# Optimization experiments

Hardware: AMD Instinct MI355X
Metric: run time of the kernel (lower is better)

The kernel has to match this reference:

```python
import jax, jax.numpy as jnp
import numpy as np
import math

D_MODEL = 1024
N_HEADS = 16
HEAD_DIM = 64
BATCH = 2
SEQ = 2048


def setup_inputs() -> dict:
    key = jax.random.key(0)
    ks = jax.random.split(key, 5)
    x = jax.random.normal(ks[0], (BATCH, SEQ, D_MODEL), dtype=jnp.float32)
    s = 0.02
    wq = jax.random.normal(ks[1], (D_MODEL, D_MODEL), dtype=jnp.float32) * s
    wk = jax.random.normal(ks[2], (D_MODEL, D_MODEL), dtype=jnp.float32) * s
    wv = jax.random.normal(ks[3], (D_MODEL, D_MODEL), dtype=jnp.float32) * s
    wo = jax.random.normal(ks[4], (D_MODEL, D_MODEL), dtype=jnp.float32) * s
    gammas = jnp.linspace(0.9, 0.99, N_HEADS, dtype=jnp.float32)
    return {"x": x, "wq": wq, "wk": wk, "wv": wv, "wo": wo, "gammas": gammas}


def _decay_mask(length: int, gammas: jnp.ndarray, dtype) -> jnp.ndarray:
    # [H, L, L]: gamma^(t-s) for t >= s, else 0 (causal exponential decay)
    pos = jnp.arange(length)
    diff = pos[:, None] - pos[None, :]
    causal = diff >= 0
    d = jnp.maximum(diff, 0).astype(dtype)
    g = gammas.astype(dtype)[:, None, None]
    return jnp.where(causal[None], jnp.power(g, d[None]), jnp.zeros((), dtype))


def reference(x, wq, wk, wv, wo, gammas):
    B, L, D = x.shape
    H, hd = N_HEADS, HEAD_DIM
    # torch nn.Linear: y = x @ W.T
    q = (x @ wq.T).reshape(B, L, H, hd)
    k = (x @ wk.T).reshape(B, L, H, hd)
    v = (x @ wv.T).reshape(B, L, H, hd)
    scale = 1.0 / math.sqrt(hd)
    scores = jnp.einsum('bthd,bshd->bhts', q * scale, k)  # [B,H,L,L]
    decay = _decay_mask(L, gammas, x.dtype)               # [H,L,L]
    weights = scores * decay[None]
    retained = jnp.einsum('bhts,bshd->bthd', weights, v)  # [B,L,H,hd]
    return retained.reshape(B, L, H * hd) @ wo.T
```

## Files before the change

### kernel.cpp

```cpp
#include <hip/hip_runtime.h>


typedef __attribute__((ext_vector_type(8))) short bf16x8;
typedef __attribute__((ext_vector_type(4))) float f32x4;
typedef __attribute__((ext_vector_type(16))) float f32x16;
typedef __attribute__((ext_vector_type(4))) unsigned short u16x4;
typedef __attribute__((ext_vector_type(8))) unsigned short u16x8;
typedef __attribute__((ext_vector_type(4))) unsigned int u32x4;

__device__ inline unsigned short f2bf(float f) {
    unsigned int u;
    __builtin_memcpy(&u, &f, 4);
    u += 0x7fffu + ((u >> 16) & 1u);
    return (unsigned short)(u >> 16);
}

__device__ inline f32x4 mfma16(bf16x8 a, bf16x8 b, f32x4 c) {
    return __builtin_amdgcn_mfma_f32_16x16x32_bf16(a, b, c, 0, 0, 0);
}
__device__ inline f32x16 mfma32(bf16x8 a, bf16x8 b, f32x16 c) {
    return __builtin_amdgcn_mfma_f32_32x32x16_bf16(a, b, c, 0, 0, 0);
}

__device__ inline void gl16(const unsigned short* g, unsigned short* l) {
    __builtin_amdgcn_global_load_lds(
        (const __attribute__((address_space(1))) unsigned int*)g,
        (__attribute__((address_space(3))) unsigned int*)l,
        16, 0, 0);
}

__device__ inline unsigned cvtpk(float lo, float hi) {
    unsigned r;
    asm("v_cvt_pk_bf16_f32 %0, %1, %2" : "=v"(r) : "v"(lo), "v"(hi));
    return r;
}

__global__ __launch_bounds__(256) void convert_bf16(
    const float* __restrict__ x,
    const float* __restrict__ wq, const float* __restrict__ wk,
    const float* __restrict__ wv, const float* __restrict__ wo,
    unsigned short* __restrict__ xb,
    unsigned short* __restrict__ wqb, unsigned short* __restrict__ wkb,
    unsigned short* __restrict__ wvb, unsigned short* __restrict__ wob)
{
    int cid = blockIdx.x * 256 + threadIdx.x;
    #pragma unroll
    for (int it = 0; it < 4; ++it, cid += 262144) {
        const float* src;
        unsigned short* dst;
        size_t off;
        if (cid < 524288) {
            src = x; dst = xb; off = (size_t)cid * 8;
        } else {
            const int t = cid - 524288;
            const int seg = t >> 17;
            off = (size_t)(t & 131071) * 8;
            src = seg == 0 ? wq : seg == 1 ? wk : seg == 2 ? wv : wo;
            dst = seg == 0 ? wqb : seg == 1 ? wkb : seg == 2 ? wvb : wob;
        }
        f32x4 a = *(const f32x4*)(src + off);
        f32x4 b = *(const f32x4*)(src + off + 4);
        u32x4 v = { cvtpk(a[0], a[1]), cvtpk(a[2], a[3]),
                    cvtpk(b[0], b[1]), cvtpk(b[2], b[3]) };
        *(u32x4*)(dst + off) = v;
    }
}

__global__ __launch_bounds__(256) void qkv_bf16(
    const unsigned short* __restrict__ xb,
    const unsigned short* __restrict__ wqb, const unsigned short* __restrict__ wkb,
    const unsigned short* __restrict__ wvb,
    unsigned short* __restrict__ qfr, unsigned short* __restrict__ kfr,
    unsigned short* __restrict__ vfr)
{
    __shared__ unsigned short sR[128 * 64];
    __shared__ unsigned short sL[128 * 64];

    const int z = blockIdx.z;
    const unsigned short* W = (z == 0) ? wqb : (z == 1) ? wkb : wvb;
    const unsigned short* Rs = (z < 2) ? xb : W;
    const unsigned short* Ls = (z < 2) ? W : xb;
    const int rblk = (z < 2) ? blockIdx.x : blockIdx.y;
    const int lblk = (z < 2) ? blockIdx.y : blockIdx.x;

    const int tid = threadIdx.x;
    const int l = tid & 63, w = tid >> 6;
    const int lrow = l & 15, koff4 = (l >> 4) * 4;
    const int swz = lrow & 7;
    const int wrow = (w >> 1) * 64, wcol = (w & 1) * 64;

    f32x4 acc[4][4] = {};

    const int srow = w * 32 + (l >> 3);
    const int scol = ((l & 7) ^ ((l >> 3) & 7)) * 8;
    const unsigned short* gR = Rs + (size_t)(rblk * 128 + srow) * 1024 + scol;
    const unsigned short* gL = Ls + (size_t)(lblk * 128 + srow) * 1024 + scol;
    unsigned short* lRb = sR + (w * 32) * 64;
    unsigned short* lLb = sL + (w * 32) * 64;

    for (int kk = 0; kk < 1024; kk += 64) {
        #pragma unroll
        for (int p = 0; p < 4; ++p) {
            gl16(gR + (size_t)p * 8 * 1024 + kk, lRb + p * 512);
            gl16(gL + (size_t)p * 8 * 1024 + kk, lLb + p * 512);
        }
        __syncthreads();
        #pragma unroll
        for (int kt = 0; kt < 2; ++kt) {
            bf16x8 aL[4], bR[4];
            #pragma unroll
            for (int f = 0; f < 4; ++f) {
                const int co = ((kt * 4 + (l >> 4)) ^ swz) * 8;
                aL[f] = *(const bf16x8*)&sL[(wcol + f * 16 + lrow) * 64 + co];
                bR[f] = *(const bf16x8*)&sR[(wrow + f * 16 + lrow) * 64 + co];
            }
            #pragma unroll
            for (int af = 0; af < 4; ++af)
                #pragma unroll
                for (int bf = 0; bf < 4; ++bf)
                    acc[af][bf] = mfma16(aL[af], bR[bf], acc[af][bf]);
        }
        __syncthreads();
    }

    #pragma unroll
    for (int af = 0; af < 4; ++af) {
        #pragma unroll
        for (int bf = 0; bf < 4; ++bf) {
            const int m = rblk * 128 + wrow + bf * 16 + lrow;
            const int n0 = lblk * 128 + wcol + af * 16 + koff4;
            f32x4 v = acc[af][bf];
            unsigned p0 = cvtpk(v[0], v[1]), p1 = cvtpk(v[2], v[3]);
            u16x4 val = { (unsigned short)(p0 & 0xffff), (unsigned short)(p0 >> 16),
                          (unsigned short)(p1 & 0xffff), (unsigned short)(p1 >> 16) };
            if (z < 2) {
                const int bq = m >> 11, s = m & 2047;
                const int h2 = n0 >> 6, dd = n0 & 63;
                const size_t addr = (size_t)((bq * 16 + h2) * 64 + (s >> 5)) * 2048
                                  + (size_t)(dd >> 4) * 512 + (size_t)((dd >> 3) & 1) * 256
                                  + (size_t)(s & 31) * 8 + (dd & 7);
                unsigned short* dst = z ? kfr : qfr;
                *(u16x4*)(dst + addr) = val;
            } else {
                const int h2 = m >> 6, dd = m & 63;
                const int bq = n0 >> 11, t = n0 & 2047;
                const size_t addr = (size_t)((bq * 16 + h2) * 64 + (t >> 5)) * 2048
                                  + (size_t)((dd >> 5) * 2 + ((t >> 4) & 1)) * 512
                                  + (size_t)((t >> 3) & 1) * 256
                                  + (size_t)(dd & 31) * 8 + (t & 7);
                *(u16x4*)(vfr + addr) = val;
            }
        }
    }
}

__global__ __launch_bounds__(256) void retention_chunked(
    const unsigned short* __restrict__ qfr, const unsigned short* __restrict__ kfr,
    const unsigned short* __restrict__ vfr, const float* __restrict__ gammas,
    unsigned short* __restrict__ ret)
{
    __shared__ float red[3][32][64];

    const int bid = blockIdx.x;
    const int xcd = bid & 7;
    const int idx = bid >> 3;
    const int bh  = (xcd << 2) | (idx & 3);
    const int tw  = 63 - (idx >> 2);
    const int b = bh >> 4, h = bh & 15;
    const float lg = log2f(gammas[h]);
    const int cut_i = (int)(45.0f / (-lg));

    const int tid = threadIdx.x;
    const int l = tid & 63, w = tid >> 6;
    const int l31 = l & 31, hi = l >> 5;
    const int tw0 = tw << 5;
    const int tq = tw0 + l31;

    const size_t hbase = (size_t)((b * 16 + h) * 64) * 2048;
    const unsigned short* qfb = qfr + hbase + l * 8;
    const unsigned short* kfb = kfr + hbase + l * 8;
    const unsigned short* vfb = vfr + hbase + l * 8;

    bf16x8 qf[4];
    #pragma unroll
    for (int kt = 0; kt < 4; ++kt)
        qf[kt] = *(const bf16x8*)(qfb + (size_t)tw * 2048 + kt * 512);

    float cf[16];
    #pragma unroll
    for (int r = 0; r < 16; ++r) {
        const int crow = (r & 3) + (hi << 2) + ((r >> 2) << 3);
        cf[r] = exp2f((float)(31 - crow) * lg);
    }

    auto ldk = [&](int sb, bf16x8* kf) {
        const unsigned short* p = kfb + (size_t)sb * 2048;
        #pragma unroll
        for (int kt = 0; kt < 4; ++kt) kf[kt] = *(const bf16x8*)(p + kt * 512);
    };
    auto ldv = [&](int sb, bf16x8* vf) {
        const unsigned short* p = vfb + (size_t)sb * 2048;
        #pragma unroll
        for (int i = 0; i < 4; ++i) vf[i] = *(const bf16x8*)(p + i * 512);
    };

    int sb_lo = tw0 - 31 - cut_i;
    sb_lo = (sb_lo <= 0) ? 0 : (sb_lo >> 5);

    const int n = tw - sb_lo + 1;
    const int chunk = (n + 3) >> 2;
    const int my_lo = sb_lo + w * chunk;
    int my_hi = my_lo + chunk;
    if (my_hi > tw + 1) my_hi = tw + 1;

    f32x16 acc0 = {}, acc1 = {};

    if (my_lo < my_hi) {
        bf16x8 kc[4], vc[4], kn[4], vn[4];
        ldk(my_lo, kc);
        ldv(my_lo, vc);

        for (int sb = my_lo; sb < my_hi; ++sb) {
            if (sb + 1 < my_hi) { ldk(sb + 1, kn); ldv(sb + 1, vn); }
            const int s0 = sb << 5;
            f32x16 sc = {};
            #pragma unroll
            for (int kt = 0; kt < 4; ++kt) sc = mfma32(kc[kt], qf[kt], sc);

            const float rowf = 0.125f * exp2f((float)(tq - s0 - 31) * lg);
            const bool diag = (sb == tw);
            const int dtq = tq - s0;
            float wv_[16];
            #pragma unroll
            for (int r = 0; r < 16; ++r) {
                float t_ = sc[r] * rowf * cf[r];
                if (diag) {
                    const int crow = (r & 3) + (hi << 2) + ((r >> 2) << 3);
                    t_ = (dtq >= crow) ? t_ : 0.0f;
                }
                wv_[r] = t_;
            }
            unsigned pk_[8];
            #pragma unroll
            for (int i = 0; i < 8; ++i) pk_[i] = cvtpk(wv_[2 * i], wv_[2 * i + 1]);
            asm("v_permlane32_swap_b32 %0, %1" : "+v"(pk_[0]), "+v"(pk_[2]));
            asm("v_permlane32_swap_b32 %0, %1" : "+v"(pk_[1]), "+v"(pk_[3]));
            asm("v_permlane32_swap_b32 %0, %1" : "+v"(pk_[4]), "+v"(pk_[6]));
            asm("v_permlane32_swap_b32 %0, %1" : "+v"(pk_[5]), "+v"(pk_[7]));
            u32x4 f0v = { pk_[0], pk_[1], pk_[2], pk_[3] };
            u32x4 f1v = { pk_[4], pk_[5], pk_[6], pk_[7] };
            const bf16x8 pa0 = __builtin_bit_cast(bf16x8, f0v);
            const bf16x8 pa1 = __builtin_bit_cast(bf16x8, f1v);
            acc0 = mfma32(pa0, vc[0], acc0);
            acc0 = mfma32(pa1, vc[1], acc0);
            acc1 = mfma32(pa0, vc[2], acc1);
            acc1 = mfma32(pa1, vc[3], acc1);

            if (sb + 1 < my_hi) {
                #pragma unroll
                for (int i = 0; i < 4; ++i) { kc[i] = kn[i]; vc[i] = vn[i]; }
            }
        }
    }

    if (w > 0) {
        #pragma unroll
        for (int r = 0; r < 16; ++r) {
            red[w - 1][r][l]      = acc0[r];
            red[w - 1][r + 16][l] = acc1[r];
        }
    }
    __syncthreads();
    if (w == 0) {
        #pragma unroll
        for (int j = 0; j < 3; ++j)
            #pragma unroll
            for (int r = 0; r < 16; ++r) {
                acc0[r] += red[j][r][l];
                acc1[r] += red[j][r + 16][l];
            }
        #pragma unroll
        for (int r = 0; r < 16; ++r) {
            const int tl = (r & 3) + (hi << 2) + ((r >> 2) << 3);
            unsigned short* dst = ret + (size_t)(b * 2048 + tw0 + tl) * 1024 + h * 64 + l31;
            dst[0]  = f2bf(acc0[r]);
            dst[32] = f2bf(acc1[r]);
        }
    }
}

__global__ __launch_bounds__(256) void out_bf16(
    const unsigned short* __restrict__ ret, const unsigned short* __restrict__ wob,
    float* __restrict__ out)
{
    __shared__ unsigned short sR[128 * 64];
    __shared__ unsigned short sL[128 * 64];

    const int rblk = blockIdx.x;
    const int lblk = blockIdx.y;

    const int tid = threadIdx.x;
    const int l = tid & 63, w = tid >> 6;
    const int lrow = l & 15, koff4 = (l >> 4) * 4;
    const int swz = lrow & 7;
    const int wrow = (w >> 1) * 64, wcol = (w & 1) * 64;

    f32x4 acc[4][4] = {};

    const int srow = w * 32 + (l >> 3);
    const int scol = ((l & 7) ^ ((l >> 3) & 7)) * 8;
    const unsigned short* gR = ret + (size_t)(rblk * 128 + srow) * 1024 + scol;
    const unsigned short* gL = wob + (size_t)(lblk * 128 + srow) * 1024 + scol;
    unsigned short* lRb = sR + (w * 32) * 64;
    unsigned short* lLb = sL + (w * 32) * 64;

    for (int kk = 0; kk < 1024; kk += 64) {
        #pragma unroll
        for (int p = 0; p < 4; ++p) {
            gl16(gR + (size_t)p * 8 * 1024 + kk, lRb + p * 512);
            gl16(gL + (size_t)p * 8 * 1024 + kk, lLb + p * 512);
        }
        __syncthreads();
        #pragma unroll
        for (int kt = 0; kt < 2; ++kt) {
            bf16x8 aL[4], bR[4];
            #pragma unroll
            for (int f = 0; f < 4; ++f) {
                const int co = ((kt * 4 + (l >> 4)) ^ swz) * 8;
                aL[f] = *(const bf16x8*)&sL[(wcol + f * 16 + lrow) * 64 + co];
                bR[f] = *(const bf16x8*)&sR[(wrow + f * 16 + lrow) * 64 + co];
            }
            #pragma unroll
            for (int af = 0; af < 4; ++af)
                #pragma unroll
                for (int bf = 0; bf < 4; ++bf)
                    acc[af][bf] = mfma16(aL[af], bR[bf], acc[af][bf]);
        }
        __syncthreads();
    }

    #pragma unroll
    for (int af = 0; af < 4; ++af)
        #pragma unroll
        for (int bf = 0; bf < 4; ++bf) {
            const int m = rblk * 128 + wrow + bf * 16 + lrow;
            const int n0 = lblk * 128 + wcol + af * 16 + koff4;
            *(f32x4*)(out + (size_t)m * 1024 + n0) = acc[af][bf];
        }
}

extern "C" void kernel_launch(void* const* d_in, const int* in_sizes, int n_in,
                              void* d_out, int out_size, void* d_ws, size_t ws_size,
                              hipStream_t stream) {
    const float* x      = (const float*)d_in[0];
    const float* wq     = (const float*)d_in[1];
    const float* wk     = (const float*)d_in[2];
    const float* wv     = (const float*)d_in[3];
    const float* wo     = (const float*)d_in[4];
    const float* gammas = (const float*)d_in[5];
    float* out = (float*)d_out;

    unsigned short* ws = (unsigned short*)d_ws;
    unsigned short* qf  = ws;
    unsigned short* kf  = ws + (size_t)4 * 1024 * 1024;
    unsigned short* vf  = ws + (size_t)8 * 1024 * 1024;
    unsigned short* ret = ws + (size_t)12 * 1024 * 1024;
    unsigned short* xb  = ret;
    unsigned short* wqb = ws + (size_t)16 * 1024 * 1024;
    unsigned short* wkb = ws + (size_t)17 * 1024 * 1024;
    unsigned short* wvb = ws + (size_t)18 * 1024 * 1024;
    unsigned short* wob = ws + (size_t)19 * 1024 * 1024;

    convert_bf16<<<1024, 256, 0, stream>>>(x, wq, wk, wv, wo, xb, wqb, wkb, wvb, wob);
    qkv_bf16<<<dim3(32, 8, 3), 256, 0, stream>>>(xb, wqb, wkb, wvb, qf, kf, vf);
    retention_chunked<<<2048, 256, 0, stream>>>(qf, kf, vf, gammas, ret);
    out_bf16<<<dim3(32, 8), 256, 0, stream>>>(ret, wob, out);
}
```

Before: 96.48 us.

## Pair causal query tiles per block to balance retention workload

Each block now processes two query tiles, 63-p and p, so the triangular causal work is balanced across blocks, and the grid is halved. The per-iteration exp2f for the row decay factor is replaced by a running multiply with gamma^-32. MFMA sections get raised wave priority, and the diagonal masking is split into its own branch. The cost is serialising two tiles per block plus an extra barrier, and some drift in the incremental decay factor.

```diff
diff --git a/kernel.cpp b/kernel.cpp
--- a/kernel.cpp
+++ b/kernel.cpp
@@ -154,7 +154,7 @@
     }
 }
 
-__global__ __launch_bounds__(256) void retention_chunked(
+__global__ __launch_bounds__(256) void retention_paired(
     const unsigned short* __restrict__ qfr, const unsigned short* __restrict__ kfr,
     const unsigned short* __restrict__ vfr, const float* __restrict__ gammas,
     unsigned short* __restrict__ ret)
@@ -163,28 +163,22 @@
 
     const int bid = blockIdx.x;
     const int xcd = bid & 7;
-    const int idx = bid >> 3;
-    const int bh  = (xcd << 2) | (idx & 3);
-    const int tw  = 63 - (idx >> 2);
+    const int j = bid >> 3;
+    const int bh  = (xcd << 2) | (j & 3);
+    const int p = j >> 2;
     const int b = bh >> 4, h = bh & 15;
     const float lg = log2f(gammas[h]);
     const int cut_i = (int)(45.0f / (-lg));
+    const float gi32 = exp2f(-32.0f * lg);
 
     const int tid = threadIdx.x;
     const int l = tid & 63, w = tid >> 6;
     const int l31 = l & 31, hi = l >> 5;
-    const int tw0 = tw << 5;
-    const int tq = tw0 + l31;
 
     const size_t hbase = (size_t)((b * 16 + h) * 64) * 2048;
     const unsigned short* qfb = qfr + hbase + l * 8;
     const unsigned short* kfb = kfr + hbase + l * 8;
     const unsigned short* vfb = vfr + hbase + l * 8;
-
-    bf16x8 qf[4];
-    #pragma unroll
-    for (int kt = 0; kt < 4; ++kt)
-        qf[kt] = *(const bf16x8*)(qfb + (size_t)tw * 2048 + kt * 512);
 
     float cf[16];
     #pragma unroll
@@ -194,99 +188,119 @@
     }
 
     auto ldk = [&](int sb, bf16x8* kf) {
-        const unsigned short* p = kfb + (size_t)sb * 2048;
-        #pragma unroll
-        for (int kt = 0; kt < 4; ++kt) kf[kt] = *(const bf16x8*)(p + kt * 512);
+        const unsigned short* ptr = kfb + (size_t)sb * 2048;
+        #pragma unroll
+        for (int kt = 0; kt < 4; ++kt) kf[kt] = *(const bf16x8*)(ptr + kt * 512);
     };
     auto ldv = [&](int sb, bf16x8* vf) {
-        const unsigned short* p = vfb + (size_t)sb * 2048;
-        #pragma unroll
-        for (int i = 0; i < 4; ++i) vf[i] = *(const bf16x8*)(p + i * 512);
+        const unsigned short* ptr = vfb + (size_t)sb * 2048;
+        #pragma unroll
+        for (int i = 0; i < 4; ++i) vf[i] = *(const bf16x8*)(ptr + i * 512);
     };
 
-    int sb_lo = tw0 - 31 - cut_i;
-    sb_lo = (sb_lo <= 0) ? 0 : (sb_lo >> 5);
-
-    const int n = tw - sb_lo + 1;
-    const int chunk = (n + 3) >> 2;
-    const int my_lo = sb_lo + w * chunk;
-    int my_hi = my_lo + chunk;
-    if (my_hi > tw + 1) my_hi = tw + 1;
-
-    f32x16 acc0 = {}, acc1 = {};
-
-    if (my_lo < my_hi) {
-        bf16x8 kc[4], vc[4], kn[4], vn[4];
-        ldk(my_lo, kc);
-        ldv(my_lo, vc);
-
-        for (int sb = my_lo; sb < my_hi; ++sb) {
-            if (sb + 1 < my_hi) { ldk(sb + 1, kn); ldv(sb + 1, vn); }
-            const int s0 = sb << 5;
-            f32x16 sc = {};
-            #pragma unroll
-            for (int kt = 0; kt < 4; ++kt) sc = mfma32(kc[kt], qf[kt], sc);
-
-            const float rowf = 0.125f * exp2f((float)(tq - s0 - 31) * lg);
-            const bool diag = (sb == tw);
-            const int dtq = tq - s0;
-            float wv_[16];
+    auto do_tile = [&](int tw) {
+        const int tw0 = tw << 5;
+        const int tq = tw0 + l31;
+
+        bf16x8 qf[4];
+        #pragma unroll
+        for (int kt = 0; kt < 4; ++kt)
+            qf[kt] = *(const bf16x8*)(qfb + (size_t)tw * 2048 + kt * 512);
+
+        int sb_lo = tw0 - 31 - cut_i;
+        sb_lo = (sb_lo <= 0) ? 0 : (sb_lo >> 5);
+
+        const int n = tw - sb_lo + 1;
+        const int chunk = (n + 3) >> 2;
+        const int my_lo = sb_lo + w * chunk;
+        int my_hi = my_lo + chunk;
+        if (my_hi > tw + 1) my_hi = tw + 1;
+
+        f32x16 acc0 = {}, acc1 = {};
+
+        if (my_lo < my_hi) {
+            float rowf = 0.125f * exp2f((float)(tq - (my_lo << 5) - 31) * lg);
+            bf16x8 kc[4], vc[4], kn[4], vn[4];
+            ldk(my_lo, kc);
+            ldv(my_lo, vc);
+
+            for (int sb = my_lo; sb < my_hi; ++sb) {
+                if (sb + 1 < my_hi) { ldk(sb + 1, kn); ldv(sb + 1, vn); }
+                f32x16 sc = {};
+                __builtin_amdgcn_s_setprio(1);
+                #pragma unroll
+                for (int kt = 0; kt < 4; ++kt) sc = mfma32(kc[kt], qf[kt], sc);
+                __builtin_amdgcn_s_setprio(0);
+
+                float wv_[16];
+                if (sb == tw) {
+                    const int dtq = tq - (sb << 5);
+                    #pragma unroll
+                    for (int r = 0; r < 16; ++r) {
+                        const int crow = (r & 3) + (hi << 2) + ((r >> 2) << 3);
+                        float t_ = sc[r] * rowf * cf[r];
+                        wv_[r] = (dtq >= crow) ? t_ : 0.0f;
+                    }
+                } else {
+                    #pragma unroll
+                    for (int r = 0; r < 16; ++r)
+                        wv_[r] = sc[r] * rowf * cf[r];
+                }
+                unsigned pk_[8];
+                #pragma unroll
+                for (int i = 0; i < 8; ++i) pk_[i] = cvtpk(wv_[2 * i], wv_[2 * i + 1]);
+                asm("v_permlane32_swap_b32 %0, %1" : "+v"(pk_[0]), "+v"(pk_[2]));
+                asm("v_permlane32_swap_b32 %0, %1" : "+v"(pk_[1]), "+v"(pk_[3]));
+                asm("v_permlane32_swap_b32 %0, %1" : "+v"(pk_[4]), "+v"(pk_[6]));
+                asm("v_permlane32_swap_b32 %0, %1" : "+v"(pk_[5]), "+v"(pk_[7]));
+                u32x4 f0v = { pk_[0], pk_[1], pk_[2], pk_[3] };
+                u32x4 f1v = { pk_[4], pk_[5], pk_[6], pk_[7] };
+                const bf16x8 pa0 = __builtin_bit_cast(bf16x8, f0v);
+                const bf16x8 pa1 = __builtin_bit_cast(bf16x8, f1v);
+                __builtin_amdgcn_s_setprio(1);
+                acc0 = mfma32(pa0, vc[0], acc0);
+                acc0 = mfma32(pa1, vc[1], acc0);
+                acc1 = mfma32(pa0, vc[2], acc1);
+                acc1 = mfma32(pa1, vc[3], acc1);
+                __builtin_amdgcn_s_setprio(0);
+
+                rowf *= gi32;
+                if (sb + 1 < my_hi) {
+                    #pragma unroll
+                    for (int i = 0; i < 4; ++i) { kc[i] = kn[i]; vc[i] = vn[i]; }
+                }
+            }
+        }
+
+        if (w > 0) {
             #pragma unroll
             for (int r = 0; r < 16; ++r) {
-                float t_ = sc[r] * rowf * cf[r];
-                if (diag) {
-                    const int crow = (r & 3) + (hi << 2) + ((r >> 2) << 3);
-                    t_ = (dtq >= crow) ? t_ : 0.0f;
+                red[w - 1][r][l]      = acc0[r];
+                red[w - 1][r + 16][l] = acc1[r];
+            }
+        }
+        __syncthreads();
+        if (w == 0) {
+            #pragma unroll
+            for (int jj = 0; jj < 3; ++jj)
+                #pragma unroll
+                for (int r = 0; r < 16; ++r) {
+                    acc0[r] += red[jj][r][l];
+                    acc1[r] += red[jj][r + 16][l];
                 }
-                wv_[r] = t_;
-            }
-            unsigned pk_[8];
-            #pragma unroll
-            for (int i = 0; i < 8; ++i) pk_[i] = cvtpk(wv_[2 * i], wv_[2 * i + 1]);
-            asm("v_permlane32_swap_b32 %0, %1" : "+v"(pk_[0]), "+v"(pk_[2]));
-            asm("v_permlane32_swap_b32 %0, %1" : "+v"(pk_[1]), "+v"(pk_[3]));
-            asm("v_permlane32_swap_b32 %0, %1" : "+v"(pk_[4]), "+v"(pk_[6]));
-            asm("v_permlane32_swap_b32 %0, %1" : "+v"(pk_[5]), "+v"(pk_[7]));
-            u32x4 f0v = { pk_[0], pk_[1], pk_[2], pk_[3] };
-            u32x4 f1v = { pk_[4], pk_[5], pk_[6], pk_[7] };
-            const bf16x8 pa0 = __builtin_bit_cast(bf16x8, f0v);
-            const bf16x8 pa1 = __builtin_bit_cast(bf16x8, f1v);
-            acc0 = mfma32(pa0, vc[0], acc0);
-            acc0 = mfma32(pa1, vc[1], acc0);
-            acc1 = mfma32(pa0, vc[2], acc1);
-            acc1 = mfma32(pa1, vc[3], acc1);
-
-            if (sb + 1 < my_hi) {
-                #pragma unroll
-                for (int i = 0; i < 4; ++i) { kc[i] = kn[i]; vc[i] = vn[i]; }
-            }
-        }
-    }
-
-    if (w > 0) {
-        #pragma unroll
-        for (int r = 0; r < 16; ++r) {
-            red[w - 1][r][l]      = acc0[r];
-            red[w - 1][r + 16][l] = acc1[r];
-        }
-    }
-    __syncthreads();
-    if (w == 0) {
-        #pragma unroll
-        for (int j = 0; j < 3; ++j)
             #pragma unroll
             for (int r = 0; r < 16; ++r) {
-                acc0[r] += red[j][r][l];
-                acc1[r] += red[j][r + 16][l];
-            }
-        #pragma unroll
-        for (int r = 0; r < 16; ++r) {
-            const int tl = (r & 3) + (hi << 2) + ((r >> 2) << 3);
-            unsigned short* dst = ret + (size_t)(b * 2048 + tw0 + tl) * 1024 + h * 64 + l31;
-            dst[0]  = f2bf(acc0[r]);
-            dst[32] = f2bf(acc1[r]);
-        }
-    }
+                const int tl = (r & 3) + (hi << 2) + ((r >> 2) << 3);
+                unsigned short* dst = ret + (size_t)(b * 2048 + tw0 + tl) * 1024 + h * 64 + l31;
+                dst[0]  = f2bf(acc0[r]);
+                dst[32] = f2bf(acc1[r]);
+            }
+        }
+        __syncthreads();
+    };
+
+    do_tile(63 - p);
+    do_tile(p);
 }
 
 __global__ __launch_bounds__(256) void out_bf16(
@@ -373,6 +387,6 @@
 
     convert_bf16<<<1024, 256, 0, stream>>>(x, wq, wk, wv, wo, xb, wqb, wkb, wvb, wob);
     qkv_bf16<<<dim3(32, 8, 3), 256, 0, stream>>>(xb, wqb, wkb, wvb, qf, kf, vf);
-    retention_chunked<<<2048, 256, 0, stream>>>(qf, kf, vf, gammas, ret);
+    retention_paired<<<1024, 256, 0, stream>>>(qf, kf, vf, gammas, ret);
     out_bf16<<<dim3(32, 8), 256, 0, stream>>>(ret, wob, out);
 }
```

New measurement: 94.60 us. Within noise of the previous version (-1.9%).
